# Kernel optimization log

Measured on AMD Instinct MI355X. Metric: run time of the kernel, lower is better.

## Reference

```python
import jax, jax.numpy as jnp
import numpy as np

K = 16  # neighbors per node


def _knn_idx(p):
    # p: [N,3] -> indices of K nearest neighbors (squared Euclidean), no self-loop
    sq = jnp.sum(p * p, axis=1)
    d2 = sq[:, None] + sq[None, :] - 2.0 * (p @ p.T)  # [N,N]
    n = p.shape[0]
    d2 = jnp.where(jnp.eye(n, dtype=bool), jnp.inf, d2)
    _, idx = jax.lax.top_k(-d2, K)  # smallest distances
    return idx  # [N,K]


def _gcn(x, nbr, W, b):
    # PyG GCNConv: symmetric-normalized A-hat = A + I. For a kNN graph every
    # node has in-degree exactly K, so deg-hat = K+1 uniformly and the norm
    # deg^-1/2[src]*deg^-1/2[dst] collapses to 1/(K+1) for every edge.
    h = x @ W  # [N,H]
    scale = 1.0 / (K + 1.0)
    agg = (jnp.sum(h[nbr], axis=1) + h) * scale  # neighbor sum + self loop
    return agg + b


def setup_inputs() -> dict:
    key = jax.random.key(0)
    ks = jax.random.split(key, 7)
    s = 0.1
    return {
        "coords": jax.random.normal(ks[0], (8, 2048, 6), jnp.float32),
        "W1": jax.random.normal(ks[1], (6, 64), jnp.float32) * s,
        "b1": jax.random.normal(ks[2], (64,), jnp.float32) * s,
        "W2": jax.random.normal(ks[3], (64, 128), jnp.float32) * s,
        "b2": jax.random.normal(ks[4], (128,), jnp.float32) * s,
        "Wf": jax.random.normal(ks[5], (128, 128), jnp.float32) * s,
        "bf": jax.random.normal(ks[6], (128,), jnp.float32) * s,
    }


def reference(coords, W1, b1, W2, b2, Wf, bf):
    def per_sample(feats):  # feats: [N,6]
        nbr = _knn_idx(feats[:, :3])
        x = jax.nn.relu(_gcn(feats, nbr, W1, b1))
        x = jax.nn.relu(_gcn(x, nbr, W2, b2))
        return x @ Wf + bf  # final Linear

    return jax.vmap(per_sample)(coords)  # [B,N,out_dim]
```

## Files before the change

### kernel.cpp

```cpp
#include <hip/hip_runtime.h>

#define NN    2048
#define KNN   16
#define BATCH 8

__device__ __forceinline__ unsigned umin_u(unsigned a, unsigned b) { return a < b ? a : b; }

__device__ __forceinline__ unsigned long long bcast64(unsigned long long v, int l) {
  unsigned lo = __builtin_amdgcn_readlane((unsigned)(v & 0xffffffffu), l);
  unsigned hi = __builtin_amdgcn_readlane((unsigned)(v >> 32), l);
  return ((unsigned long long)hi << 32) | lo;
}

__device__ __forceinline__ unsigned long long dpp_shr1_zero(unsigned long long v) {
  int lo = __builtin_amdgcn_update_dpp(0, (int)(unsigned)(v & 0xffffffffu), 0x111, 0xf, 0xf, true);
  int hi = __builtin_amdgcn_update_dpp(0, (int)(unsigned)(v >> 32),        0x111, 0xf, 0xf, true);
  return ((unsigned long long)(unsigned)hi << 32) | (unsigned)lo;
}

__global__ __launch_bounds__(512) void knn_l1_kernel(const float* __restrict__ coords,
                                                     const float* __restrict__ W1,
                                                     const float* __restrict__ b1,
                                                     int* __restrict__ nbr,
                                                     float* __restrict__ x1) {
  __shared__ float4 sP[NN];

  const int b        = blockIdx.x >> 8;
  const int nodeBase = (blockIdx.x & 255) << 3;
  const int lane     = (int)threadIdx.x & 63;
  const int wid      = (int)threadIdx.x >> 6;

  const float* cb = coords + (size_t)b * NN * 6;
  for (int p = threadIdx.x; p < NN; p += 512) {
    const float2 v01 = *reinterpret_cast<const float2*>(cb + p * 6);
    const float2 v23 = *reinterpret_cast<const float2*>(cb + p * 6 + 2);
    float4 v; v.x = v01.x; v.y = v01.y; v.z = v23.x;
    v.w = v.x * v.x + v.y * v.y + v.z * v.z;
    sP[p] = v;
  }
  __syncthreads();

  const int i = nodeBase + wid;
  const float4 pi = sP[i];

  float lmin = 1e30f;
  for (int t0 = 0; t0 < NN; t0 += 64) {
    const float4 pj = sP[t0 + lane];
    const float d2 = (pi.w + pj.w) - 2.0f * (pi.x * pj.x + pi.y * pj.y + pi.z * pj.z);
    lmin = fminf(lmin, d2);
  }
  unsigned lm = __float_as_uint(lmin);
  lm = lm ^ (unsigned)((((int)lm) >> 31) | 0x80000000);

  unsigned tau = 0u;
  for (int bit = 31; bit >= 0; --bit) {
    const unsigned t_try = tau + ((1u << bit) - 1u);
    const unsigned long long m = __ballot(lm <= t_try);
    if (__popcll(m) < 17) tau += (1u << bit);
  }
  const unsigned tau_s = (tau >= 0xFFFFFFC0u) ? 0xFFFFFFFFu : tau + 64u;

  unsigned long long lk  = ~0ull;
  unsigned long long kth = ((unsigned long long)tau_s << 32) | 0xFFFFFFFFull;

  for (int attempt = 0; attempt < 2; ++attempt) {
    for (int t0 = 0; t0 < NN; t0 += 64) {
      const int j = t0 + lane;
      const float4 pj = sP[j];
      const float d2 = (pi.w + pj.w) - 2.0f * (pi.x * pj.x + pi.y * pj.y + pi.z * pj.z);
      unsigned u   = __float_as_uint(d2);
      unsigned k32 = u ^ (unsigned)((((int)u) >> 31) | 0x80000000);
      const unsigned long long ck = ((unsigned long long)k32 << 32) | (unsigned)j;

      unsigned long long mask = __ballot(ck < kth && j != i);
      while (mask) {
        const int src = __ffsll((unsigned long long)mask) - 1;
        mask &= mask - 1;
        const unsigned long long c = bcast64(ck, src);
        if (c < kth) {
          const unsigned long long pk = dpp_shr1_zero(lk);
          lk = (lk < c) ? lk : (pk < c ? c : pk);
          const unsigned long long nk = bcast64(lk, 15);
          kth = (nk < kth) ? nk : kth;
        }
      }
    }
    if (bcast64(lk, 15) != ~0ull) break;
    lk = ~0ull; kth = ~0ull;
  }

  const int nj = (int)umin_u((unsigned)(lk & 0xffffffffu), NN - 1u);
  if (lane < KNN) {
    nbr[((size_t)b * NN + i) * KNN + lane] = nj;
  }

  float r[6];
#pragma unroll
  for (int c = 0; c < 6; ++c) r[c] = 0.f;
  if (lane < KNN) {
    const float* row = cb + (size_t)nj * 6;
    const float2 a = *reinterpret_cast<const float2*>(row);
    const float2 m = *reinterpret_cast<const float2*>(row + 2);
    const float2 q = *reinterpret_cast<const float2*>(row + 4);
    r[0] = a.x; r[1] = a.y; r[2] = m.x; r[3] = m.y; r[4] = q.x; r[5] = q.y;
  }
#pragma unroll
  for (int m = 1; m <= 8; m <<= 1) {
#pragma unroll
    for (int c = 0; c < 6; ++c) r[c] += __shfl_xor(r[c], m);
  }
  const float* self = cb + (size_t)i * 6;
  float agg[6];
#pragma unroll
  for (int c = 0; c < 6; ++c) {
    const float nbs = __uint_as_float(__builtin_amdgcn_readfirstlane(__float_as_uint(r[c])));
    agg[c] = (nbs + self[c]) * (1.0f / 17.0f);
  }
  float acc = b1[lane];
#pragma unroll
  for (int c = 0; c < 6; ++c) acc = fmaf(agg[c], W1[c * 64 + lane], acc);
  x1[((size_t)b * NN + i) * 64 + lane] = fmaxf(acc, 0.f);
}

__global__ __launch_bounds__(256) void layers_kernel(const float* __restrict__ x1,
                                                     const int* __restrict__ nbr,
                                                     const float* __restrict__ W2,
                                                     const float* __restrict__ b2,
                                                     const float* __restrict__ Wf,
                                                     const float* __restrict__ bf,
                                                     float* __restrict__ out) {
  __shared__ float sA[32][68];
  __shared__ float sB[32][132];
  __shared__ int   sN[512];

  const int t        = (int)threadIdx.x;
  const int nodeBase = blockIdx.x * 32;
  const int bs       = nodeBase >> 11;

  sN[t]       = (int)umin_u((unsigned)nbr[(size_t)nodeBase * KNN + t],       NN - 1u);
  sN[t + 256] = (int)umin_u((unsigned)nbr[(size_t)nodeBase * KNN + t + 256], NN - 1u);
  __syncthreads();

  {
    const int ln = t >> 3;
    const int d8 = (t & 7) * 8;
    const int n  = nodeBase + ln;
    const float* Xb = x1 + (((size_t)bs) << 11) * 64;
    const float* xn = x1 + (size_t)n * 64 + d8;
    float4 s0 = *reinterpret_cast<const float4*>(xn);
    float4 s1 = *reinterpret_cast<const float4*>(xn + 4);
    const int* nb = &sN[ln * 16];
#pragma unroll
    for (int k = 0; k < KNN; ++k) {
      const float* row = Xb + (size_t)nb[k] * 64 + d8;
      const float4 v0 = *reinterpret_cast<const float4*>(row);
      const float4 v1 = *reinterpret_cast<const float4*>(row + 4);
      s0.x += v0.x; s0.y += v0.y; s0.z += v0.z; s0.w += v0.w;
      s1.x += v1.x; s1.y += v1.y; s1.z += v1.z; s1.w += v1.w;
    }
    const float sc = 1.0f / 17.0f;
    sA[ln][d8 + 0] = s0.x * sc; sA[ln][d8 + 1] = s0.y * sc;
    sA[ln][d8 + 2] = s0.z * sc; sA[ln][d8 + 3] = s0.w * sc;
    sA[ln][d8 + 4] = s1.x * sc; sA[ln][d8 + 5] = s1.y * sc;
    sA[ln][d8 + 6] = s1.z * sc; sA[ln][d8 + 7] = s1.w * sc;
  }
  __syncthreads();

  const int ng = (t >> 5) * 4;
  const int o4 = (t & 31) * 4;

  {
    const float4 bv = *reinterpret_cast<const float4*>(b2 + o4);
    float4 acc0 = bv, acc1 = bv, acc2 = bv, acc3 = bv;
#pragma unroll 4
    for (int c = 0; c < 64; ++c) {
      const float4 w = *reinterpret_cast<const float4*>(W2 + (size_t)c * 128 + o4);
      const float a0 = sA[ng + 0][c];
      const float a1 = sA[ng + 1][c];
      const float a2 = sA[ng + 2][c];
      const float a3 = sA[ng + 3][c];
      acc0.x += a0 * w.x; acc0.y += a0 * w.y; acc0.z += a0 * w.z; acc0.w += a0 * w.w;
      acc1.x += a1 * w.x; acc1.y += a1 * w.y; acc1.z += a1 * w.z; acc1.w += a1 * w.w;
      acc2.x += a2 * w.x; acc2.y += a2 * w.y; acc2.z += a2 * w.z; acc2.w += a2 * w.w;
      acc3.x += a3 * w.x; acc3.y += a3 * w.y; acc3.z += a3 * w.z; acc3.w += a3 * w.w;
    }
    sB[ng + 0][o4 + 0] = fmaxf(acc0.x, 0.f); sB[ng + 0][o4 + 1] = fmaxf(acc0.y, 0.f);
    sB[ng + 0][o4 + 2] = fmaxf(acc0.z, 0.f); sB[ng + 0][o4 + 3] = fmaxf(acc0.w, 0.f);
    sB[ng + 1][o4 + 0] = fmaxf(acc1.x, 0.f); sB[ng + 1][o4 + 1] = fmaxf(acc1.y, 0.f);
    sB[ng + 1][o4 + 2] = fmaxf(acc1.z, 0.f); sB[ng + 1][o4 + 3] = fmaxf(acc1.w, 0.f);
    sB[ng + 2][o4 + 0] = fmaxf(acc2.x, 0.f); sB[ng + 2][o4 + 1] = fmaxf(acc2.y, 0.f);
    sB[ng + 2][o4 + 2] = fmaxf(acc2.z, 0.f); sB[ng + 2][o4 + 3] = fmaxf(acc2.w, 0.f);
    sB[ng + 3][o4 + 0] = fmaxf(acc3.x, 0.f); sB[ng + 3][o4 + 1] = fmaxf(acc3.y, 0.f);
    sB[ng + 3][o4 + 2] = fmaxf(acc3.z, 0.f); sB[ng + 3][o4 + 3] = fmaxf(acc3.w, 0.f);
  }
  __syncthreads();

  {
    const float4 bv = *reinterpret_cast<const float4*>(bf + o4);
    float4 acc0 = bv, acc1 = bv, acc2 = bv, acc3 = bv;
#pragma unroll 4
    for (int c = 0; c < 128; ++c) {
      const float4 w = *reinterpret_cast<const float4*>(Wf + (size_t)c * 128 + o4);
      const float a0 = sB[ng + 0][c];
      const float a1 = sB[ng + 1][c];
      const float a2 = sB[ng + 2][c];
      const float a3 = sB[ng + 3][c];
      acc0.x += a0 * w.x; acc0.y += a0 * w.y; acc0.z += a0 * w.z; acc0.w += a0 * w.w;
      acc1.x += a1 * w.x; acc1.y += a1 * w.y; acc1.z += a1 * w.z; acc1.w += a1 * w.w;
      acc2.x += a2 * w.x; acc2.y += a2 * w.y; acc2.z += a2 * w.z; acc2.w += a2 * w.w;
      acc3.x += a3 * w.x; acc3.y += a3 * w.y; acc3.z += a3 * w.z; acc3.w += a3 * w.w;
    }
    float* o0 = out + (size_t)(nodeBase + ng) * 128 + o4;
    *reinterpret_cast<float4*>(o0)           = acc0;
    *reinterpret_cast<float4*>(o0 + 128)     = acc1;
    *reinterpret_cast<float4*>(o0 + 256)     = acc2;
    *reinterpret_cast<float4*>(o0 + 384)     = acc3;
  }
}

extern "C" void kernel_launch(void* const* d_in, const int* in_sizes, int n_in,
                              void* d_out, int out_size, void* d_ws, size_t ws_size,
                              hipStream_t stream) {
  const float* coords = (const float*)d_in[0];
  const float* W1 = (const float*)d_in[1];
  const float* b1 = (const float*)d_in[2];
  const float* W2 = (const float*)d_in[3];
  const float* b2 = (const float*)d_in[4];
  const float* Wf = (const float*)d_in[5];
  const float* bf = (const float*)d_in[6];
  float* out = (float*)d_out;

  char* ws = (char*)d_ws;
  int*   nbr = (int*)ws;
  float* x1  = (float*)(ws + (size_t)(1u << 20) * 1);

  knn_l1_kernel<<<BATCH * (NN / 8), 512, 0, stream>>>(coords, W1, b1, nbr, x1);

  layers_kernel<<<(BATCH * NN) / 32, 256, 0, stream>>>(x1, nbr, W2, b2, Wf, bf, out);
}
```

Measured before the change: 123.4 us.

## Cache kNN distance keys in registers and double per-block node tile in layers kernel

The kNN kernel now computes each lane's 32 distance keys once, keeps them in a register array, and reuses them in the selection pass instead of recomputing distances from LDS. The initial threshold drops the +64 slack, so it is tighter. The layers kernel processes 64 nodes per block with 8 nodes per thread and consumes two weight rows per step, raising weight reuse per global load. In exchange, register pressure rises in both kernels (32 keys plus the k-list state, and 8 float4 accumulators), which can lower occupancy. The grid for the layers kernel is halved.

```diff
diff --git a/kernel.cpp b/kernel.cpp
--- a/kernel.cpp
+++ b/kernel.cpp
@@ -43,35 +43,33 @@
   const int i = nodeBase + wid;
   const float4 pi = sP[i];
 
-  float lmin = 1e30f;
-  for (int t0 = 0; t0 < NN; t0 += 64) {
-    const float4 pj = sP[t0 + lane];
+  unsigned key[32];
+  unsigned lmin = 0xFFFFFFFFu;
+#pragma unroll
+  for (int it = 0; it < 32; ++it) {
+    const float4 pj = sP[(it << 6) + lane];
     const float d2 = (pi.w + pj.w) - 2.0f * (pi.x * pj.x + pi.y * pj.y + pi.z * pj.z);
-    lmin = fminf(lmin, d2);
-  }
-  unsigned lm = __float_as_uint(lmin);
-  lm = lm ^ (unsigned)((((int)lm) >> 31) | 0x80000000);
+    unsigned u   = __float_as_uint(d2);
+    unsigned k32 = u ^ (unsigned)((((int)u) >> 31) | 0x80000000);
+    key[it] = k32;
+    lmin = umin_u(lmin, k32);
+  }
 
   unsigned tau = 0u;
   for (int bit = 31; bit >= 0; --bit) {
     const unsigned t_try = tau + ((1u << bit) - 1u);
-    const unsigned long long m = __ballot(lm <= t_try);
+    const unsigned long long m = __ballot(lmin <= t_try);
     if (__popcll(m) < 17) tau += (1u << bit);
   }
-  const unsigned tau_s = (tau >= 0xFFFFFFC0u) ? 0xFFFFFFFFu : tau + 64u;
 
   unsigned long long lk  = ~0ull;
-  unsigned long long kth = ((unsigned long long)tau_s << 32) | 0xFFFFFFFFull;
+  unsigned long long kth = ((unsigned long long)tau << 32) | 0xFFFFFFFFull;
 
   for (int attempt = 0; attempt < 2; ++attempt) {
-    for (int t0 = 0; t0 < NN; t0 += 64) {
-      const int j = t0 + lane;
-      const float4 pj = sP[j];
-      const float d2 = (pi.w + pj.w) - 2.0f * (pi.x * pj.x + pi.y * pj.y + pi.z * pj.z);
-      unsigned u   = __float_as_uint(d2);
-      unsigned k32 = u ^ (unsigned)((((int)u) >> 31) | 0x80000000);
-      const unsigned long long ck = ((unsigned long long)k32 << 32) | (unsigned)j;
-
+#pragma unroll
+    for (int it = 0; it < 32; ++it) {
+      const int j = (it << 6) + lane;
+      const unsigned long long ck = ((unsigned long long)key[it] << 32) | (unsigned)j;
       unsigned long long mask = __ballot(ck < kth && j != i);
       while (mask) {
         const int src = __ffsll((unsigned long long)mask) - 1;
@@ -129,92 +127,100 @@
                                                      const float* __restrict__ Wf,
                                                      const float* __restrict__ bf,
                                                      float* __restrict__ out) {
-  __shared__ float sA[32][68];
-  __shared__ float sB[32][132];
-  __shared__ int   sN[512];
+  __shared__ float sA[64][68];
+  __shared__ float sB[64][132];
+  __shared__ int   sN[1024];
 
   const int t        = (int)threadIdx.x;
-  const int nodeBase = blockIdx.x * 32;
+  const int nodeBase = blockIdx.x * 64;
   const int bs       = nodeBase >> 11;
 
-  sN[t]       = (int)umin_u((unsigned)nbr[(size_t)nodeBase * KNN + t],       NN - 1u);
-  sN[t + 256] = (int)umin_u((unsigned)nbr[(size_t)nodeBase * KNN + t + 256], NN - 1u);
+#pragma unroll
+  for (int q = 0; q < 4; ++q)
+    sN[t + q * 256] = (int)umin_u((unsigned)nbr[(size_t)nodeBase * KNN + t + q * 256], NN - 1u);
   __syncthreads();
 
   {
-    const int ln = t >> 3;
-    const int d8 = (t & 7) * 8;
+    const int ln = t >> 2;
+    const int d0 = (t & 3) * 16;
     const int n  = nodeBase + ln;
     const float* Xb = x1 + (((size_t)bs) << 11) * 64;
-    const float* xn = x1 + (size_t)n * 64 + d8;
+    const float* xn = x1 + (size_t)n * 64 + d0;
     float4 s0 = *reinterpret_cast<const float4*>(xn);
     float4 s1 = *reinterpret_cast<const float4*>(xn + 4);
+    float4 s2 = *reinterpret_cast<const float4*>(xn + 8);
+    float4 s3 = *reinterpret_cast<const float4*>(xn + 12);
     const int* nb = &sN[ln * 16];
 #pragma unroll
     for (int k = 0; k < KNN; ++k) {
-      const float* row = Xb + (size_t)nb[k] * 64 + d8;
+      const float* row = Xb + (size_t)nb[k] * 64 + d0;
       const float4 v0 = *reinterpret_cast<const float4*>(row);
       const float4 v1 = *reinterpret_cast<const float4*>(row + 4);
+      const float4 v2 = *reinterpret_cast<const float4*>(row + 8);
+      const float4 v3 = *reinterpret_cast<const float4*>(row + 12);
       s0.x += v0.x; s0.y += v0.y; s0.z += v0.z; s0.w += v0.w;
       s1.x += v1.x; s1.y += v1.y; s1.z += v1.z; s1.w += v1.w;
+      s2.x += v2.x; s2.y += v2.y; s2.z += v2.z; s2.w += v2.w;
+      s3.x += v3.x; s3.y += v3.y; s3.z += v3.z; s3.w += v3.w;
     }
     const float sc = 1.0f / 17.0f;
-    sA[ln][d8 + 0] = s0.x * sc; sA[ln][d8 + 1] = s0.y * sc;
-    sA[ln][d8 + 2] = s0.z * sc; sA[ln][d8 + 3] = s0.w * sc;
-    sA[ln][d8 + 4] = s1.x * sc; sA[ln][d8 + 5] = s1.y * sc;
-    sA[ln][d8 + 6] = s1.z * sc; sA[ln][d8 + 7] = s1.w * sc;
-  }
-  __syncthreads();
-
-  const int ng = (t >> 5) * 4;
+    float* dst = &sA[ln][d0];
+    dst[0]  = s0.x * sc; dst[1]  = s0.y * sc; dst[2]  = s0.z * sc; dst[3]  = s0.w * sc;
+    dst[4]  = s1.x * sc; dst[5]  = s1.y * sc; dst[6]  = s1.z * sc; dst[7]  = s1.w * sc;
+    dst[8]  = s2.x * sc; dst[9]  = s2.y * sc; dst[10] = s2.z * sc; dst[11] = s2.w * sc;
+    dst[12] = s3.x * sc; dst[13] = s3.y * sc; dst[14] = s3.z * sc; dst[15] = s3.w * sc;
+  }
+  __syncthreads();
+
+  const int ng = (t >> 5) * 8;
   const int o4 = (t & 31) * 4;
 
   {
     const float4 bv = *reinterpret_cast<const float4*>(b2 + o4);
-    float4 acc0 = bv, acc1 = bv, acc2 = bv, acc3 = bv;
+    float4 a0 = bv, a1 = bv, a2 = bv, a3 = bv, a4 = bv, a5 = bv, a6 = bv, a7 = bv;
 #pragma unroll 4
-    for (int c = 0; c < 64; ++c) {
-      const float4 w = *reinterpret_cast<const float4*>(W2 + (size_t)c * 128 + o4);
-      const float a0 = sA[ng + 0][c];
-      const float a1 = sA[ng + 1][c];
-      const float a2 = sA[ng + 2][c];
-      const float a3 = sA[ng + 3][c];
-      acc0.x += a0 * w.x; acc0.y += a0 * w.y; acc0.z += a0 * w.z; acc0.w += a0 * w.w;
-      acc1.x += a1 * w.x; acc1.y += a1 * w.y; acc1.z += a1 * w.z; acc1.w += a1 * w.w;
-      acc2.x += a2 * w.x; acc2.y += a2 * w.y; acc2.z += a2 * w.z; acc2.w += a2 * w.w;
-      acc3.x += a3 * w.x; acc3.y += a3 * w.y; acc3.z += a3 * w.z; acc3.w += a3 * w.w;
-    }
-    sB[ng + 0][o4 + 0] = fmaxf(acc0.x, 0.f); sB[ng + 0][o4 + 1] = fmaxf(acc0.y, 0.f);
-    sB[ng + 0][o4 + 2] = fmaxf(acc0.z, 0.f); sB[ng + 0][o4 + 3] = fmaxf(acc0.w, 0.f);
-    sB[ng + 1][o4 + 0] = fmaxf(acc1.x, 0.f); sB[ng + 1][o4 + 1] = fmaxf(acc1.y, 0.f);
-    sB[ng + 1][o4 + 2] = fmaxf(acc1.z, 0.f); sB[ng + 1][o4 + 3] = fmaxf(acc1.w, 0.f);
-    sB[ng + 2][o4 + 0] = fmaxf(acc2.x, 0.f); sB[ng + 2][o4 + 1] = fmaxf(acc2.y, 0.f);
-    sB[ng + 2][o4 + 2] = fmaxf(acc2.z, 0.f); sB[ng + 2][o4 + 3] = fmaxf(acc2.w, 0.f);
-    sB[ng + 3][o4 + 0] = fmaxf(acc3.x, 0.f); sB[ng + 3][o4 + 1] = fmaxf(acc3.y, 0.f);
-    sB[ng + 3][o4 + 2] = fmaxf(acc3.z, 0.f); sB[ng + 3][o4 + 3] = fmaxf(acc3.w, 0.f);
+    for (int c = 0; c < 64; c += 2) {
+      const float4 wA = *reinterpret_cast<const float4*>(W2 + (size_t)c * 128 + o4);
+      const float4 wB = *reinterpret_cast<const float4*>(W2 + (size_t)(c + 1) * 128 + o4);
+#define STEP_B(q, acc) { const float2 a = *reinterpret_cast<const float2*>(&sA[ng + q][c]); \
+      acc.x += a.x * wA.x + a.y * wB.x; acc.y += a.x * wA.y + a.y * wB.y;                   \
+      acc.z += a.x * wA.z + a.y * wB.z; acc.w += a.x * wA.w + a.y * wB.w; }
+      STEP_B(0, a0) STEP_B(1, a1) STEP_B(2, a2) STEP_B(3, a3)
+      STEP_B(4, a4) STEP_B(5, a5) STEP_B(6, a6) STEP_B(7, a7)
+#undef STEP_B
+    }
+#define STORE_B(q, acc) { float* d = &sB[ng + q][o4];                        \
+    d[0] = fmaxf(acc.x, 0.f); d[1] = fmaxf(acc.y, 0.f);                      \
+    d[2] = fmaxf(acc.z, 0.f); d[3] = fmaxf(acc.w, 0.f); }
+    STORE_B(0, a0) STORE_B(1, a1) STORE_B(2, a2) STORE_B(3, a3)
+    STORE_B(4, a4) STORE_B(5, a5) STORE_B(6, a6) STORE_B(7, a7)
+#undef STORE_B
   }
   __syncthreads();
 
   {
     const float4 bv = *reinterpret_cast<const float4*>(bf + o4);
-    float4 acc0 = bv, acc1 = bv, acc2 = bv, acc3 = bv;
+    float4 a0 = bv, a1 = bv, a2 = bv, a3 = bv, a4 = bv, a5 = bv, a6 = bv, a7 = bv;
 #pragma unroll 4
-    for (int c = 0; c < 128; ++c) {
-      const float4 w = *reinterpret_cast<const float4*>(Wf + (size_t)c * 128 + o4);
-      const float a0 = sB[ng + 0][c];
-      const float a1 = sB[ng + 1][c];
-      const float a2 = sB[ng + 2][c];
-      const float a3 = sB[ng + 3][c];
-      acc0.x += a0 * w.x; acc0.y += a0 * w.y; acc0.z += a0 * w.z; acc0.w += a0 * w.w;
-      acc1.x += a1 * w.x; acc1.y += a1 * w.y; acc1.z += a1 * w.z; acc1.w += a1 * w.w;
-      acc2.x += a2 * w.x; acc2.y += a2 * w.y; acc2.z += a2 * w.z; acc2.w += a2 * w.w;
-      acc3.x += a3 * w.x; acc3.y += a3 * w.y; acc3.z += a3 * w.z; acc3.w += a3 * w.w;
+    for (int c = 0; c < 128; c += 2) {
+      const float4 wA = *reinterpret_cast<const float4*>(Wf + (size_t)c * 128 + o4);
+      const float4 wB = *reinterpret_cast<const float4*>(Wf + (size_t)(c + 1) * 128 + o4);
+#define STEP_C(q, acc) { const float2 a = *reinterpret_cast<const float2*>(&sB[ng + q][c]); \
+      acc.x += a.x * wA.x + a.y * wB.x; acc.y += a.x * wA.y + a.y * wB.y;                   \
+      acc.z += a.x * wA.z + a.y * wB.z; acc.w += a.x * wA.w + a.y * wB.w; }
+      STEP_C(0, a0) STEP_C(1, a1) STEP_C(2, a2) STEP_C(3, a3)
+      STEP_C(4, a4) STEP_C(5, a5) STEP_C(6, a6) STEP_C(7, a7)
+#undef STEP_C
     }
     float* o0 = out + (size_t)(nodeBase + ng) * 128 + o4;
-    *reinterpret_cast<float4*>(o0)           = acc0;
-    *reinterpret_cast<float4*>(o0 + 128)     = acc1;
-    *reinterpret_cast<float4*>(o0 + 256)     = acc2;
-    *reinterpret_cast<float4*>(o0 + 384)     = acc3;
+    *reinterpret_cast<float4*>(o0)       = a0;
+    *reinterpret_cast<float4*>(o0 + 128) = a1;
+    *reinterpret_cast<float4*>(o0 + 256) = a2;
+    *reinterpret_cast<float4*>(o0 + 384) = a3;
+    *reinterpret_cast<float4*>(o0 + 512) = a4;
+    *reinterpret_cast<float4*>(o0 + 640) = a5;
+    *reinterpret_cast<float4*>(o0 + 768) = a6;
+    *reinterpret_cast<float4*>(o0 + 896) = a7;
   }
 }
 
@@ -236,5 +242,5 @@
 
   knn_l1_kernel<<<BATCH * (NN / 8), 512, 0, stream>>>(coords, W1, b1, nbr, x1);
 
-  layers_kernel<<<(BATCH * NN) / 32, 256, 0, stream>>>(x1, nbr, W2, b2, Wf, bf, out);
-}
+  layers_kernel<<<(BATCH * NN) / 64, 256, 0, stream>>>(x1, nbr, W2, b2, Wf, bf, out);
+}
```

Measured after the change: 127.5 us. 1.03x slower.
